# Kernel tuning notes

Hardware: AMD Instinct MI355X
Metric: run time of the kernel (lower is better)

Reference implementation:

```python
import jax, jax.numpy as jnp
import numpy as np

D_MODEL = 512
STATE_DIM = 64
INNER = 768  # ceil(512 * 1.5)
KERNEL = 3
EPS = 1e-5
DELTA_MIN = 1e-4
DELTA_MAX = 3.0


def _hippo_legS(n):
    A = np.zeros((n, n), dtype=np.float32)
    for i in range(n):
        ci = np.sqrt(2 * i + 1)
        for m in range(i + 1):
            cm = np.sqrt(2 * m + 1)
            if i == m:
                A[i, m] = -(2 * i + 1)
            else:
                sign = -1.0 if (i - m) % 2 == 0 else 1.0
                A[i, m] = sign * ci * cm
    idx = np.arange(n, dtype=np.float32)
    B = np.sqrt(2.0 * idx + 1.0)
    C = B.copy()
    C[1::2] *= -1.0
    return A, B, C


def setup_inputs() -> dict:
    key = jax.random.key(0)
    k1, k2, k3, k4 = jax.random.split(key, 4)
    x = jax.random.normal(k1, (8, 2048, D_MODEL), dtype=jnp.float32)
    norm_w = jnp.ones((D_MODEL,), jnp.float32)
    norm_b = jnp.zeros((D_MODEL,), jnp.float32)
    W_in = jax.random.normal(k2, (D_MODEL, 3 * INNER), jnp.float32) * 0.02
    conv_w = jax.random.normal(k3, (INNER, KERNEL), jnp.float32) * 0.2  # torch (C,1,k) squeezed
    A_np, B_np, C_np = _hippo_legS(STATE_DIM)
    scale = 1.0 / np.sqrt(INNER)
    A = jnp.asarray(A_np)
    B_mat = jnp.asarray(np.repeat(B_np[:, None], INNER, axis=1) * scale)   # [N, inner]
    C_mat = jnp.asarray(np.repeat(C_np[None, :], INNER, axis=0) * scale)   # [inner, N]
    W_out = jax.random.normal(k4, (INNER, D_MODEL), jnp.float32) * 0.02
    return {"x": x, "norm_w": norm_w, "norm_b": norm_b, "W_in": W_in,
            "conv_w": conv_w, "A": A, "B_mat": B_mat, "C_mat": C_mat, "W_out": W_out}


def reference(x, norm_w, norm_b, W_in, conv_w, A, B_mat, C_mat, W_out):
    Bsz, L, D = x.shape
    N = A.shape[0]
    # LayerNorm (biased variance, as torch)
    mu = x.mean(-1, keepdims=True)
    var = jnp.mean((x - mu) ** 2, axis=-1, keepdims=True)
    h = (x - mu) / jnp.sqrt(var + EPS) * norm_w + norm_b
    proj = h @ W_in                                 # [B, L, 3*inner]
    data, gate, delta_raw = jnp.split(proj, 3, axis=-1)
    # causal depthwise conv: torch pads k-1 both sides then truncates to L
    k = conv_w.shape[1]
    xp = jnp.pad(data, ((0, 0), (k - 1, 0), (0, 0)))
    kern = conv_w.T[:, None, :]                     # [k, 1, inner] (WIO)
    conv = jax.lax.conv_general_dilated(
        xp, kern, window_strides=(1,), padding='VALID',
        dimension_numbers=('NWC', 'WIO', 'NWC'), feature_group_count=INNER)
    u = jax.nn.silu(conv)                           # [B, L, inner]
    delta = jnp.minimum(jax.nn.softplus(delta_raw).mean(-1) + DELTA_MIN, DELTA_MAX)  # [B, L]
    I = jnp.eye(N, dtype=x.dtype)

    def step(state, inp):
        u_t, dt = inp                               # [B, inner], [B]
        Bu = jnp.einsum('nd,bd->bn', B_mat, u_t)    # [B, N]
        rhs = state + dt[:, None] * Bu
        mat = I - dt[:, None, None] * A             # [B, N, N]
        st = jnp.linalg.solve(mat, rhs[..., None])[..., 0]
        y = jnp.einsum('dn,bn->bd', C_mat, st)      # [B, inner]
        return st, y

    state0 = jnp.zeros((Bsz, N), x.dtype)
    _, ys = jax.lax.scan(step, state0, (jnp.swapaxes(u, 0, 1), delta.T))
    selective = jnp.swapaxes(ys, 0, 1)              # [B, L, inner]
    gated = jax.nn.sigmoid(gate) * selective
    return x + gated @ W_out
```

## Files before the change

### kernel.cpp

```cpp
#include <hip/hip_runtime.h>

typedef unsigned short u16;
typedef short short8 __attribute__((ext_vector_type(8)));
typedef float f32x4 __attribute__((ext_vector_type(4)));

#define D_MODEL 512
#define INNER 768
#define N3 2304
#define LSEQ 2048
#define BATCH 8
#define MROWS 16384

constexpr size_t OFF_H     = 0;
constexpr size_t OFF_WINT  = 16777216;
constexpr size_t OFF_WOUTT = 19136512;
constexpr size_t OFF_DATA  = 19922944;
constexpr size_t OFF_GATE  = 45088768;
constexpr size_t OFF_DSUM  = 70254592;
constexpr size_t OFF_YBAR  = 70451200;
constexpr size_t WS_NEEDED = 70516736;

__device__ __forceinline__ u16 f2bf(float f) {
  unsigned u = __builtin_bit_cast(unsigned, f);
  u += 0x7fffu + ((u >> 16) & 1u);
  return (u16)(u >> 16);
}
__device__ __forceinline__ float bf2f(u16 h) {
  unsigned u = ((unsigned)h) << 16;
  return __builtin_bit_cast(float, u);
}

__device__ __forceinline__ float dpp_shr1(float x) {
  int r = __builtin_amdgcn_update_dpp(0, __builtin_bit_cast(int, x),
                                      0x138 , 0xf, 0xf, true);
  return __builtin_bit_cast(float, r);
}

#if __has_builtin(__builtin_amdgcn_global_load_lds)
#define HAVE_GLLDS 1
__device__ __forceinline__ void gl_lds16(const u16* g, u16* l) {
  __builtin_amdgcn_global_load_lds(
      (const __attribute__((address_space(1))) unsigned int*)g,
      (__attribute__((address_space(3))) unsigned int*)l, 16, 0, 0);
}
#else
#define HAVE_GLLDS 0
#endif

__global__ __launch_bounds__(256) void transp_cast(const float* __restrict__ in,
                                                   u16* __restrict__ out, int R, int C) {
  __shared__ float tile[32][33];
  int c0 = blockIdx.x * 32, r0 = blockIdx.y * 32;
  int tx = threadIdx.x, ty = threadIdx.y;
#pragma unroll
  for (int i = 0; i < 4; ++i)
    tile[ty + i * 8][tx] = in[(size_t)(r0 + ty + i * 8) * C + c0 + tx];
  __syncthreads();
#pragma unroll
  for (int i = 0; i < 4; ++i)
    out[(size_t)(c0 + ty + i * 8) * R + r0 + tx] = f2bf(tile[tx][ty + i * 8]);
}

__global__ __launch_bounds__(256) void ln_kernel(const float* __restrict__ x,
                                                 const float* __restrict__ gw,
                                                 const float* __restrict__ gb,
                                                 u16* __restrict__ h) {
  int row = blockIdx.x * 4 + (threadIdx.x >> 6);
  int lane = threadIdx.x & 63;
  const float* xr = x + (size_t)row * D_MODEL;
  float4 v0 = *(const float4*)(xr + lane * 4);
  float4 v1 = *(const float4*)(xr + 256 + lane * 4);
  float s  = v0.x + v0.y + v0.z + v0.w + v1.x + v1.y + v1.z + v1.w;
  float s2 = v0.x * v0.x + v0.y * v0.y + v0.z * v0.z + v0.w * v0.w +
             v1.x * v1.x + v1.y * v1.y + v1.z * v1.z + v1.w * v1.w;
#pragma unroll
  for (int m = 1; m < 64; m <<= 1) { s += __shfl_xor(s, m); s2 += __shfl_xor(s2, m); }
  float mu = s * (1.0f / 512.0f);
  float var = s2 * (1.0f / 512.0f) - mu * mu;
  float rstd = rsqrtf(var + 1e-5f);
  float4 w0 = *(const float4*)(gw + lane * 4);
  float4 w1 = *(const float4*)(gw + 256 + lane * 4);
  float4 b0 = *(const float4*)(gb + lane * 4);
  float4 b1 = *(const float4*)(gb + 256 + lane * 4);
  float y0 = (v0.x - mu) * rstd * w0.x + b0.x;
  float y1 = (v0.y - mu) * rstd * w0.y + b0.y;
  float y2 = (v0.z - mu) * rstd * w0.z + b0.z;
  float y3 = (v0.w - mu) * rstd * w0.w + b0.w;
  float y4 = (v1.x - mu) * rstd * w1.x + b1.x;
  float y5 = (v1.y - mu) * rstd * w1.y + b1.y;
  float y6 = (v1.z - mu) * rstd * w1.z + b1.z;
  float y7 = (v1.w - mu) * rstd * w1.w + b1.w;
  uint2 pa, pb;
  pa.x = (unsigned)f2bf(y0) | ((unsigned)f2bf(y1) << 16);
  pa.y = (unsigned)f2bf(y2) | ((unsigned)f2bf(y3) << 16);
  pb.x = (unsigned)f2bf(y4) | ((unsigned)f2bf(y5) << 16);
  pb.y = (unsigned)f2bf(y6) | ((unsigned)f2bf(y7) << 16);
  *(uint2*)(h + (size_t)row * D_MODEL + lane * 4) = pa;
  *(uint2*)(h + (size_t)row * D_MODEL + 256 + lane * 4) = pb;
}

template <int MODE, int XT>
__global__ __launch_bounds__(256) void gemm_bt(
    const u16* __restrict__ A, const u16* __restrict__ BT, int K,
    u16* __restrict__ dataBuf, u16* __restrict__ gateSig, float* __restrict__ deltaSum,
    const float* __restrict__ ybarp, const float* __restrict__ xres,
    float* __restrict__ outp) {
  __shared__ u16 As[128 * 32];
  __shared__ u16 Bs[128 * 32];
  int bi = blockIdx.x;
  int xcd = bi & 7, s = bi >> 3;
  int m0 = (xcd * 16 + s / XT) * 128;
  int n0 = (s % XT) * 128;

  int tid = threadIdx.x;
  int lane = tid & 63, wv = tid >> 6;
  int wm = wv >> 1, wn = wv & 1;
  f32x4 acc[4][4];
#pragma unroll
  for (int i = 0; i < 4; ++i)
#pragma unroll
    for (int j = 0; j < 4; ++j) acc[i][j] = (f32x4)0.0f;

  int r4 = tid >> 2;
  int c4 = (((tid & 3) ^ ((tid >> 3) & 3))) * 8;
  int nsteps = K >> 5;
  int mrow = wm * 64 + (lane & 15);
  int nrow = wn * 64 + (lane & 15);
  int kq = (((lane >> 4) ^ (((lane & 15) >> 1) & 3))) * 8;

  const u16* Ab = A + (size_t)(m0 + r4) * K + c4;
  const u16* Bb = BT + (size_t)(n0 + r4) * K + c4;
  const size_t rowA = (size_t)64 * K, rowB = (size_t)64 * K;
  u16* lA0 = &As[tid * 8];
  u16* lA1 = &As[(tid + 256) * 8];
  u16* lB0 = &Bs[tid * 8];
  u16* lB1 = &Bs[(tid + 256) * 8];

  for (int step = 0; step < nsteps; ++step) {
    int k0 = step * 32;
    __syncthreads();
#if HAVE_GLLDS
    gl_lds16(Ab + k0, lA0);
    gl_lds16(Ab + k0 + rowA, lA1);
    gl_lds16(Bb + k0, lB0);
    gl_lds16(Bb + k0 + rowB, lB1);
#else
    uint4 a0 = *(const uint4*)(Ab + k0);
    uint4 a1 = *(const uint4*)(Ab + k0 + rowA);
    uint4 b0 = *(const uint4*)(Bb + k0);
    uint4 b1 = *(const uint4*)(Bb + k0 + rowB);
    *(uint4*)lA0 = a0; *(uint4*)lA1 = a1;
    *(uint4*)lB0 = b0; *(uint4*)lB1 = b1;
#endif
    __syncthreads();
    short8 af[4], bfr[4];
#pragma unroll
    for (int mt = 0; mt < 4; ++mt)
      af[mt] = *(const short8*)(&As[(mrow + mt * 16) * 32 + kq]);
#pragma unroll
    for (int nt = 0; nt < 4; ++nt)
      bfr[nt] = *(const short8*)(&Bs[(nrow + nt * 16) * 32 + kq]);
#pragma unroll
    for (int mt = 0; mt < 4; ++mt)
#pragma unroll
      for (int nt = 0; nt < 4; ++nt)
        acc[mt][nt] = __builtin_amdgcn_mfma_f32_16x16x32_bf16(af[mt], bfr[nt], acc[mt][nt], 0, 0, 0);
  }

  if (MODE == 1) {
    int region = (n0 >= 1536) ? 2 : (n0 >= 768 ? 1 : 0);
    if (region < 2) {
      u16* dst = (region == 0) ? dataBuf : gateSig;
#pragma unroll
      for (int mt = 0; mt < 4; ++mt) {
        int rbase = m0 + wm * 64 + mt * 16 + (lane >> 4) * 4;
#pragma unroll
        for (int nt = 0; nt < 4; ++nt) {
          int col = n0 - region * 768 + wn * 64 + nt * 16 + (lane & 15);
#pragma unroll
          for (int r = 0; r < 4; ++r) {
            float val = acc[mt][nt][r];
            if (region == 1) val = 1.0f / (1.0f + __expf(-val));
            dst[(size_t)(rbase + r) * INNER + col] = f2bf(val);
          }
        }
      }
    } else {
#pragma unroll
      for (int mt = 0; mt < 4; ++mt) {
        int rbase = m0 + wm * 64 + mt * 16 + (lane >> 4) * 4;
        float sums[4] = {0.f, 0.f, 0.f, 0.f};
#pragma unroll
        for (int nt = 0; nt < 4; ++nt)
#pragma unroll
          for (int r = 0; r < 4; ++r) {
            float xv = acc[mt][nt][r];
            sums[r] += fmaxf(xv, 0.0f) + __logf(1.0f + __expf(-fabsf(xv)));
          }
#pragma unroll
        for (int r = 0; r < 4; ++r) {
          float val = sums[r];
          val += __shfl_xor(val, 1); val += __shfl_xor(val, 2);
          val += __shfl_xor(val, 4); val += __shfl_xor(val, 8);
          if ((lane & 15) == 0) atomicAdd(&deltaSum[rbase + r], val);
        }
      }
    }
  } else {
#pragma unroll
    for (int mt = 0; mt < 4; ++mt) {
      int rbase = m0 + wm * 64 + mt * 16 + (lane >> 4) * 4;
#pragma unroll
      for (int r = 0; r < 4; ++r) {
        float yr = ybarp[rbase + r] * 0.036084391824351615f;
#pragma unroll
        for (int nt = 0; nt < 4; ++nt) {
          int col = n0 + wn * 64 + nt * 16 + (lane & 15);
          size_t o = (size_t)(rbase + r) * D_MODEL + col;
          outp[o] = xres[o] + yr * acc[mt][nt][r];
        }
      }
    }
  }
}

__global__ __launch_bounds__(256) void conv_reduce(const u16* __restrict__ dataBuf,
                                                   const float* __restrict__ conv_w,
                                                   const float* __restrict__ deltaSum,
                                                   float2* __restrict__ pairsG) {
  int r = blockIdx.x;
  int b = r >> 11;
  int t = r & (LSEQ - 1);
  int tid = threadIdx.x;
  float part = 0.0f;
#pragma unroll
  for (int j = 0; j < 3; ++j) {
    int d = tid + j * 256;
    float cw0 = conv_w[d * 3 + 0], cw1 = conv_w[d * 3 + 1], cw2 = conv_w[d * 3 + 2];
    float x2 = bf2f(dataBuf[(size_t)r * INNER + d]);
    float x1 = (t >= 1) ? bf2f(dataBuf[(size_t)(r - 1) * INNER + d]) : 0.0f;
    float x0 = (t >= 2) ? bf2f(dataBuf[(size_t)(r - 2) * INNER + d]) : 0.0f;
    float c = cw0 * x0 + cw1 * x1 + cw2 * x2;
    part += c / (1.0f + __expf(-c));
  }
#pragma unroll
  for (int m = 1; m < 64; m <<= 1) part += __shfl_xor(part, m);
  __shared__ float red[4];
  if ((tid & 63) == 0) red[tid >> 6] = part;
  __syncthreads();
  if (tid == 0) {
    float tot = red[0] + red[1] + red[2] + red[3];
    float v = 0.036084391824351615f * tot;
    float dt = fminf(deltaSum[r] * (1.0f / 768.0f) + 1e-4f, 3.0f);
    pairsG[b * 2240 + 64 + t] = make_float2(dt, dt * v);
  }
  if (tid == 64 && t < 64)   pairsG[b * 2240 + t] = make_float2(0.f, 0.f);
  if (tid == 128 && t < 128) pairsG[b * 2240 + 2112 + t] = make_float2(0.f, 0.f);
}

__global__ __launch_bounds__(64) void ssm_scan(const float2* __restrict__ pairsG,
                                               float* __restrict__ ybar) {
  const int b = blockIdx.x;
  const int lane = threadIdx.x;
  const float2* pb = pairsG + b * 2240 + 64 - lane;
  float* yb = ybar + b * LSEQ;

  const float ddi = 2.0f * lane + 1.0f;
  const float ci = sqrtf(ddi);
  const float di = (lane & 1) ? -ci : ci;

  float2 buf[64];
#pragma unroll
  for (int j = 0; j < 32; ++j) buf[j] = pb[j];

  float P = 0.0f;
  float R = buf[0].y * ci;

  for (int blk = 0; blk < 33; ++blk) {
    int colli = 0;
    const float2* pl = pb + blk * 64 + 32;
#pragma unroll
    for (int u = 0; u < 64; ++u) {
      const int s1 = (u + 1) & 63;
      const int sl = (u + 32) & 63;
      float dt = buf[u].x;
      float gn = buf[s1].y * ci;
      float denom = fmaf(dt, ddi, 1.0f);
      float rr = __builtin_amdgcn_rcpf(denom);
      float rdi = rr * di;
      float rdiR = rdi * R;
      float dtdi = dt * di;
      float Pin = dpp_shr1(P);
      P = fmaf(rr, Pin, rdiR);
      float t1 = fmaf(-dtdi, Pin, R);
      R = fmaf(rr, t1, gn);
      int pv = __builtin_amdgcn_readlane(__builtin_bit_cast(int, P), 63);
      colli = (lane == u) ? pv : colli;
      buf[sl] = pl[u];
    }
    int t_store = blk * 64 - 63 + lane;
    if ((unsigned)t_store < (unsigned)LSEQ)
      yb[t_store] = __builtin_bit_cast(float, colli);
  }
}

extern "C" void kernel_launch(void* const* d_in, const int* in_sizes, int n_in,
                              void* d_out, int out_size, void* d_ws, size_t ws_size,
                              hipStream_t stream) {
  const float* x      = (const float*)d_in[0];
  const float* norm_w = (const float*)d_in[1];
  const float* norm_b = (const float*)d_in[2];
  const float* W_in   = (const float*)d_in[3];
  const float* conv_w = (const float*)d_in[4];
  const float* W_out  = (const float*)d_in[8];
  float* out = (float*)d_out;
  if (ws_size < WS_NEEDED) return;

  char* ws = (char*)d_ws;
  u16* h        = (u16*)(ws + OFF_H);
  u16* WinT     = (u16*)(ws + OFF_WINT);
  u16* WoutT    = (u16*)(ws + OFF_WOUTT);
  u16* dataBuf  = (u16*)(ws + OFF_DATA);
  u16* gateSig  = (u16*)(ws + OFF_GATE);
  float* dSum   = (float*)(ws + OFF_DSUM);
  float* ybar   = (float*)(ws + OFF_YBAR);
  float2* pairsG = (float2*)(ws + OFF_H);

  (void)hipMemsetAsync(dSum, 0, MROWS * sizeof(float), stream);
  transp_cast<<<dim3(N3 / 32, D_MODEL / 32), dim3(32, 8), 0, stream>>>(W_in, WinT, D_MODEL, N3);
  transp_cast<<<dim3(D_MODEL / 32, INNER / 32), dim3(32, 8), 0, stream>>>(W_out, WoutT, INNER, D_MODEL);
  ln_kernel<<<MROWS / 4, 256, 0, stream>>>(x, norm_w, norm_b, h);
  gemm_bt<1, 18><<<18 * 128, 256, 0, stream>>>(
      h, WinT, D_MODEL, dataBuf, gateSig, dSum, nullptr, nullptr, nullptr);
  conv_reduce<<<MROWS, 256, 0, stream>>>(dataBuf, conv_w, dSum, pairsG);
  ssm_scan<<<BATCH, 64, 0, stream>>>(pairsG, ybar);
  gemm_bt<2, 4><<<4 * 128, 256, 0, stream>>>(
      gateSig, WoutT, INNER, nullptr, nullptr, nullptr, ybar, x, out);
}
```

Before: 300.0 us.

## Double-buffer GEMM LDS tiles and collect scan outputs via DPP rotate

The GEMM main loop now uses two LDS buffers, so the global-to-LDS load of the next K tile is issued before the MFMAs on the current tile, removing one barrier per step and overlapping load latency with compute. The loop assumes an even number of K steps. The SSM scan replaces a per-step readlane plus lane-select with a DPP rotate and shift chain that carries lane 63's output into a register shift queue, and the store index is adjusted to match. This shortens the serial dependency chain in the scan, at the cost of doubled LDS use in the GEMM, which may lower occupancy.

```diff
diff --git a/kernel.cpp b/kernel.cpp
--- a/kernel.cpp
+++ b/kernel.cpp
@@ -33,6 +33,11 @@
 __device__ __forceinline__ float dpp_shr1(float x) {
   int r = __builtin_amdgcn_update_dpp(0, __builtin_bit_cast(int, x),
                                       0x138 , 0xf, 0xf, true);
+  return __builtin_bit_cast(float, r);
+}
+__device__ __forceinline__ float dpp_ror1(float x) {
+  int r = __builtin_amdgcn_update_dpp(0, __builtin_bit_cast(int, x),
+                                      0x13C , 0xf, 0xf, false);
   return __builtin_bit_cast(float, r);
 }
 
@@ -105,8 +110,8 @@
     u16* __restrict__ dataBuf, u16* __restrict__ gateSig, float* __restrict__ deltaSum,
     const float* __restrict__ ybarp, const float* __restrict__ xres,
     float* __restrict__ outp) {
-  __shared__ u16 As[128 * 32];
-  __shared__ u16 Bs[128 * 32];
+  __shared__ u16 As[2][128 * 32];
+  __shared__ u16 Bs[2][128 * 32];
   int bi = blockIdx.x;
   int xcd = bi & 7, s = bi >> 3;
   int m0 = (xcd * 16 + s / XT) * 128;
@@ -131,40 +136,45 @@
   const u16* Ab = A + (size_t)(m0 + r4) * K + c4;
   const u16* Bb = BT + (size_t)(n0 + r4) * K + c4;
   const size_t rowA = (size_t)64 * K, rowB = (size_t)64 * K;
-  u16* lA0 = &As[tid * 8];
-  u16* lA1 = &As[(tid + 256) * 8];
-  u16* lB0 = &Bs[tid * 8];
-  u16* lB1 = &Bs[(tid + 256) * 8];
-
-  for (int step = 0; step < nsteps; ++step) {
-    int k0 = step * 32;
-    __syncthreads();
+
+  auto stage = [&](int k0, int pbuf) {
 #if HAVE_GLLDS
-    gl_lds16(Ab + k0, lA0);
-    gl_lds16(Ab + k0 + rowA, lA1);
-    gl_lds16(Bb + k0, lB0);
-    gl_lds16(Bb + k0 + rowB, lB1);
+    gl_lds16(Ab + k0, &As[pbuf][tid * 8]);
+    gl_lds16(Ab + k0 + rowA, &As[pbuf][(tid + 256) * 8]);
+    gl_lds16(Bb + k0, &Bs[pbuf][tid * 8]);
+    gl_lds16(Bb + k0 + rowB, &Bs[pbuf][(tid + 256) * 8]);
 #else
     uint4 a0 = *(const uint4*)(Ab + k0);
     uint4 a1 = *(const uint4*)(Ab + k0 + rowA);
     uint4 b0 = *(const uint4*)(Bb + k0);
     uint4 b1 = *(const uint4*)(Bb + k0 + rowB);
-    *(uint4*)lA0 = a0; *(uint4*)lA1 = a1;
-    *(uint4*)lB0 = b0; *(uint4*)lB1 = b1;
+    *(uint4*)(&As[pbuf][tid * 8]) = a0; *(uint4*)(&As[pbuf][(tid + 256) * 8]) = a1;
+    *(uint4*)(&Bs[pbuf][tid * 8]) = b0; *(uint4*)(&Bs[pbuf][(tid + 256) * 8]) = b1;
 #endif
-    __syncthreads();
+  };
+  auto compute = [&](int pbuf) {
     short8 af[4], bfr[4];
 #pragma unroll
     for (int mt = 0; mt < 4; ++mt)
-      af[mt] = *(const short8*)(&As[(mrow + mt * 16) * 32 + kq]);
+      af[mt] = *(const short8*)(&As[pbuf][(mrow + mt * 16) * 32 + kq]);
 #pragma unroll
     for (int nt = 0; nt < 4; ++nt)
-      bfr[nt] = *(const short8*)(&Bs[(nrow + nt * 16) * 32 + kq]);
+      bfr[nt] = *(const short8*)(&Bs[pbuf][(nrow + nt * 16) * 32 + kq]);
 #pragma unroll
     for (int mt = 0; mt < 4; ++mt)
 #pragma unroll
       for (int nt = 0; nt < 4; ++nt)
         acc[mt][nt] = __builtin_amdgcn_mfma_f32_16x16x32_bf16(af[mt], bfr[nt], acc[mt][nt], 0, 0, 0);
+  };
+
+  stage(0, 0);
+  for (int step = 0; step < nsteps; step += 2) {
+    __syncthreads();
+    stage((step + 1) * 32, 1);
+    compute(0);
+    __syncthreads();
+    if (step + 2 < nsteps) stage((step + 2) * 32, 0);
+    compute(1);
   }
 
   if (MODE == 1) {
@@ -268,6 +278,7 @@
   const float ddi = 2.0f * lane + 1.0f;
   const float ci = sqrtf(ddi);
   const float di = (lane & 1) ? -ci : ci;
+  const bool lane0 = (lane == 0);
 
   float2 buf[64];
 #pragma unroll
@@ -275,9 +286,9 @@
 
   float P = 0.0f;
   float R = buf[0].y * ci;
+  float Y = 0.0f;
 
   for (int blk = 0; blk < 33; ++blk) {
-    int colli = 0;
     const float2* pl = pb + blk * 64 + 32;
 #pragma unroll
     for (int u = 0; u < 64; ++u) {
@@ -294,13 +305,14 @@
       P = fmaf(rr, Pin, rdiR);
       float t1 = fmaf(-dtdi, Pin, R);
       R = fmaf(rr, t1, gn);
-      int pv = __builtin_amdgcn_readlane(__builtin_bit_cast(int, P), 63);
-      colli = (lane == u) ? pv : colli;
+      float Pror = dpp_ror1(P);
+      float Yshr = dpp_shr1(Y);
+      Y = lane0 ? Pror : Yshr;
       buf[sl] = pl[u];
     }
-    int t_store = blk * 64 - 63 + lane;
+    int t_store = blk * 64 - lane;
     if ((unsigned)t_store < (unsigned)LSEQ)
-      yb[t_store] = __builtin_bit_cast(float, colli);
+      yb[t_store] = Y;
   }
 }
 
```

Result: no change. 298.5 us (-0.5%).

## Rescale SSM scan recurrence, shift outputs via DPP, merge transposes and memset

Applied to the files above, without the earlier changes.

Merges the two weight transpose-cast launches into one kernel and moves zeroing of the delta-sum buffer into the layernorm kernel, removing a memset and a launch. The serial SSM scan recurrence is rescaled so the per-step update needs fewer multiplies (no sqrt-scaled coefficients). The per-step readlane/select used to collect outputs is replaced by a DPP rotate-and-shift register pipeline, which changes the output index mapping. This shortens the latency-bound dependency chain of the single-wave-per-batch scan, but it relies on the rescaled algebra and the new store indexing being exactly equivalent.

```diff
diff --git a/kernel.cpp b/kernel.cpp
--- a/kernel.cpp
+++ b/kernel.cpp
@@ -35,6 +35,11 @@
                                       0x138 , 0xf, 0xf, true);
   return __builtin_bit_cast(float, r);
 }
+__device__ __forceinline__ float dpp_ror1(float x) {
+  int r = __builtin_amdgcn_update_dpp(0, __builtin_bit_cast(int, x),
+                                      0x13C , 0xf, 0xf, false);
+  return __builtin_bit_cast(float, r);
+}
 
 #if __has_builtin(__builtin_amdgcn_global_load_lds)
 #define HAVE_GLLDS 1
@@ -47,10 +52,21 @@
 #define HAVE_GLLDS 0
 #endif
 
-__global__ __launch_bounds__(256) void transp_cast(const float* __restrict__ in,
-                                                   u16* __restrict__ out, int R, int C) {
+__global__ __launch_bounds__(256) void transp2(const float* __restrict__ Wi,
+                                               u16* __restrict__ WiT,
+                                               const float* __restrict__ Wo,
+                                               u16* __restrict__ WoT) {
   __shared__ float tile[32][33];
-  int c0 = blockIdx.x * 32, r0 = blockIdx.y * 32;
+  int bi = blockIdx.x;
+  const float* in; u16* out; int R, C, c0, r0;
+  if (bi < 1152) {
+    in = Wi; out = WiT; R = D_MODEL; C = N3;
+    c0 = (bi % 72) * 32; r0 = (bi / 72) * 32;
+  } else {
+    int bj = bi - 1152;
+    in = Wo; out = WoT; R = INNER; C = D_MODEL;
+    c0 = (bj & 15) * 32; r0 = (bj >> 4) * 32;
+  }
   int tx = threadIdx.x, ty = threadIdx.y;
 #pragma unroll
   for (int i = 0; i < 4; ++i)
@@ -64,7 +80,10 @@
 __global__ __launch_bounds__(256) void ln_kernel(const float* __restrict__ x,
                                                  const float* __restrict__ gw,
                                                  const float* __restrict__ gb,
-                                                 u16* __restrict__ h) {
+                                                 u16* __restrict__ h,
+                                                 float* __restrict__ dSum) {
+  int g = blockIdx.x * 256 + threadIdx.x;
+  if (g < MROWS) dSum[g] = 0.0f;
   int row = blockIdx.x * 4 + (threadIdx.x >> 6);
   int lane = threadIdx.x & 63;
   const float* xr = x + (size_t)row * D_MODEL;
@@ -266,41 +285,41 @@
   float* yb = ybar + b * LSEQ;
 
   const float ddi = 2.0f * lane + 1.0f;
-  const float ci = sqrtf(ddi);
-  const float di = (lane & 1) ? -ci : ci;
+  const float cg = (lane & 1) ? -ddi : ddi;
+  const bool lane0 = (lane == 0);
 
   float2 buf[64];
 #pragma unroll
   for (int j = 0; j < 32; ++j) buf[j] = pb[j];
 
   float P = 0.0f;
-  float R = buf[0].y * ci;
+  float Q = buf[0].y * cg;
+  float Y = 0.0f;
 
   for (int blk = 0; blk < 33; ++blk) {
-    int colli = 0;
     const float2* pl = pb + blk * 64 + 32;
 #pragma unroll
     for (int u = 0; u < 64; ++u) {
       const int s1 = (u + 1) & 63;
       const int sl = (u + 32) & 63;
       float dt = buf[u].x;
-      float gn = buf[s1].y * ci;
+      float gq = buf[s1].y * cg;
       float denom = fmaf(dt, ddi, 1.0f);
       float rr = __builtin_amdgcn_rcpf(denom);
-      float rdi = rr * di;
-      float rdiR = rdi * R;
-      float dtdi = dt * di;
+      float dm1 = denom - 1.0f;
       float Pin = dpp_shr1(P);
-      P = fmaf(rr, Pin, rdiR);
-      float t1 = fmaf(-dtdi, Pin, R);
-      R = fmaf(rr, t1, gn);
-      int pv = __builtin_amdgcn_readlane(__builtin_bit_cast(int, P), 63);
-      colli = (lane == u) ? pv : colli;
+      float spq = Pin + Q;
+      P = rr * spq;
+      float t2 = fmaf(-dm1, Pin, Q);
+      Q = fmaf(rr, t2, gq);
+      float Pror = dpp_ror1(P);
+      float Yshr = dpp_shr1(Y);
+      Y = lane0 ? Pror : Yshr;
       buf[sl] = pl[u];
     }
-    int t_store = blk * 64 - 63 + lane;
+    int t_store = blk * 64 - lane;
     if ((unsigned)t_store < (unsigned)LSEQ)
-      yb[t_store] = __builtin_bit_cast(float, colli);
+      yb[t_store] = Y;
   }
 }
 
@@ -326,10 +345,8 @@
   float* ybar   = (float*)(ws + OFF_YBAR);
   float2* pairsG = (float2*)(ws + OFF_H);
 
-  (void)hipMemsetAsync(dSum, 0, MROWS * sizeof(float), stream);
-  transp_cast<<<dim3(N3 / 32, D_MODEL / 32), dim3(32, 8), 0, stream>>>(W_in, WinT, D_MODEL, N3);
-  transp_cast<<<dim3(D_MODEL / 32, INNER / 32), dim3(32, 8), 0, stream>>>(W_out, WoutT, INNER, D_MODEL);
-  ln_kernel<<<MROWS / 4, 256, 0, stream>>>(x, norm_w, norm_b, h);
+  transp2<<<1536, dim3(32, 8), 0, stream>>>(W_in, WinT, W_out, WoutT);
+  ln_kernel<<<MROWS / 4, 256, 0, stream>>>(x, norm_w, norm_b, h, dSum);
   gemm_bt<1, 18><<<18 * 128, 256, 0, stream>>>(
       h, WinT, D_MODEL, dataBuf, gateSig, dSum, nullptr, nullptr, nullptr);
   conv_reduce<<<MROWS, 256, 0, stream>>>(dataBuf, conv_w, dSum, pairsG);
```

Measured after the change: 288.4 us. -3.9%, faster.
